# Kernel optimization log

Hardware: AMD Instinct MI355X
Metric: run time of the kernel (lower is better)

The kernel has to match this reference:

```python
import jax, jax.numpy as jnp
import numpy as np

B, SC, SV = 32, 300, 300
D, H, L, E, F = 512, 8, 6, 6, 1024
SEM = 768
VF = SEM + 1 + 1 + 6  # semantic + scene_offset + motion + emotion(6) = 776
CHORD, ROOT, ATTR = 159, 14, 14


def _ln(x, g, b, eps=1e-5):
    m = x.mean(-1, keepdims=True)
    v = ((x - m) ** 2).mean(-1, keepdims=True)
    return (x - m) / jnp.sqrt(v + eps) * g + b


def _mha(q_in, kv_in, qkv_w, qkv_b, ow, ob, mask=None):
    d = q_in.shape[-1]
    hd = d // H
    q = (q_in @ qkv_w[:d].T + qkv_b[:d]).reshape(q_in.shape[0], q_in.shape[1], H, hd)
    k = (kv_in @ qkv_w[d:2 * d].T + qkv_b[d:2 * d]).reshape(kv_in.shape[0], kv_in.shape[1], H, hd)
    v = (kv_in @ qkv_w[2 * d:].T + qkv_b[2 * d:]).reshape(kv_in.shape[0], kv_in.shape[1], H, hd)
    s = jnp.einsum('bqhd,bkhd->bhqk', q, k) / jnp.sqrt(jnp.asarray(hd, q.dtype))
    if mask is not None:
        s = s + mask
    a = jax.nn.softmax(s, axis=-1)
    o = jnp.einsum('bhqk,bkhd->bqhd', a, v).reshape(q_in.shape)
    return o @ ow.T + ob


def _moe(x, gw, gb, w1, b1, w2, b2, w3, b3):
    # top-2 routing over E experts, SwiGLU experts (GLUExpert)
    probs = jax.nn.softmax(x @ gw.T + gb, axis=-1)  # [B,S,E]
    topv, topi = jax.lax.top_k(probs, 2)
    wts = topv / topv.sum(-1, keepdims=True)
    full = (jax.nn.one_hot(topi, E, dtype=x.dtype) * wts[..., None]).sum(-2)  # [B,S,E]
    h = jax.nn.silu(jnp.einsum('bsd,edf->bsef', x, w1) + b1) * (jnp.einsum('bsd,edf->bsef', x, w2) + b2)
    eo = jnp.einsum('bsef,efd->bsed', h, w3) + b3
    return jnp.einsum('bse,bsed->bsd', full, eo)


def reference(x, x_root, x_attr, fsem, fkey, fscene, fmotion, femotion, emb_root, emb_attr, w_chord, b_chord, w_vis, b_vis, pos_c, pos_v, enc_qkv_w, enc_qkv_b, enc_ow, enc_ob, enc_ln1_g, enc_ln1_b, enc_ln2_g, enc_ln2_b, enc_gw, enc_gb, enc_w1, enc_b1, enc_w2, enc_b2, enc_w3, enc_b3, enc_fg, enc_fb, dec_sqkv_w, dec_sqkv_b, dec_sow, dec_sob, dec_cqkv_w, dec_cqkv_b, dec_cow, dec_cob, dec_ln1_g, dec_ln1_b, dec_ln2_g, dec_ln2_b, dec_ln3_g, dec_ln3_b, dec_gw, dec_gb, dec_w1, dec_b1, dec_w2, dec_b2, dec_w3, dec_b3, dec_fg, dec_fb, wout, bout):
    Bq, S = x_root.shape
    xe = emb_root[x_root] + emb_attr[x_attr]  # chord root + attr embeddings
    keyp = jnp.broadcast_to(fkey[:, 0][:, None, None], (Bq, S, 1)).astype(xe.dtype)
    xf = jnp.concatenate([xe, keyp], -1) @ w_chord.T + b_chord
    vfc = jnp.concatenate([fsem, fscene[..., None], fmotion[..., None], femotion], -1)  # [B,Sv,VF]
    vf = vfc @ w_vis.T + b_vis
    xf = xf + pos_c[:S][None]
    vf = vf + pos_v[:vf.shape[1]][None]
    causal = jnp.where(jnp.tril(jnp.ones((S, S), bool)), 0.0, jnp.finfo(xf.dtype).min).astype(xf.dtype)
    # encoder (post-norm): self-attn -> add&norm -> MoE -> add&norm
    h = vf
    for i in range(L):
        a = _mha(h, h, enc_qkv_w[i], enc_qkv_b[i], enc_ow[i], enc_ob[i])
        h = _ln(h + a, enc_ln1_g[i], enc_ln1_b[i])
        m = _moe(h, enc_gw[i], enc_gb[i], enc_w1[i], enc_b1[i], enc_w2[i], enc_b2[i], enc_w3[i], enc_b3[i])
        h = _ln(h + m, enc_ln2_g[i], enc_ln2_b[i])
    mem = _ln(h, enc_fg, enc_fb)
    # decoder: masked self-attn, cross-attn, MoE, each add&norm
    h = xf
    for i in range(L):
        a = _mha(h, h, dec_sqkv_w[i], dec_sqkv_b[i], dec_sow[i], dec_sob[i], causal)
        h = _ln(h + a, dec_ln1_g[i], dec_ln1_b[i])
        c = _mha(h, mem, dec_cqkv_w[i], dec_cqkv_b[i], dec_cow[i], dec_cob[i])
        h = _ln(h + c, dec_ln2_g[i], dec_ln2_b[i])
        m = _moe(h, dec_gw[i], dec_gb[i], dec_w1[i], dec_b1[i], dec_w2[i], dec_b2[i], dec_w3[i], dec_b3[i])
        h = _ln(h + m, dec_ln3_g[i], dec_ln3_b[i])
    h = _ln(h, dec_fg, dec_fb)
    return h @ wout.T + bout


def setup_inputs():
    key = jax.random.key(0)
    ks = iter(jax.random.split(key, 256))
    def nrm(*s):
        return jax.random.normal(next(ks), s, jnp.float32) * 0.02
    d = {}
    d['x'] = jax.random.randint(next(ks), (B, SC), 0, CHORD)
    d['x_root'] = jax.random.randint(next(ks), (B, SC), 0, ROOT)
    d['x_attr'] = jax.random.randint(next(ks), (B, SC), 0, ATTR)
    d['fsem'] = jax.random.normal(next(ks), (B, SV, SEM), jnp.float32)
    d['fkey'] = jax.random.uniform(next(ks), (B, 1), jnp.float32)
    d['fscene'] = jax.random.uniform(next(ks), (B, SV), jnp.float32)
    d['fmotion'] = jax.random.uniform(next(ks), (B, SV), jnp.float32)
    d['femotion'] = jax.random.uniform(next(ks), (B, SV, 6), jnp.float32)
    d['emb_root'] = nrm(ROOT, D)
    d['emb_attr'] = nrm(ATTR, D)
    d['w_chord'] = nrm(D, D + 1)
    d['b_chord'] = jnp.zeros((D,), jnp.float32)
    d['w_vis'] = nrm(D, VF)
    d['b_vis'] = jnp.zeros((D,), jnp.float32)
    d['pos_c'] = nrm(SC, D)
    d['pos_v'] = nrm(SV, D)
    def attn_params(pfx_qkv, pfx_o):
        d[pfx_qkv + '_w'] = nrm(L, 3 * D, D)
        d[pfx_qkv + '_b'] = jnp.zeros((L, 3 * D), jnp.float32)
        d[pfx_o + 'w'] = nrm(L, D, D)
        d[pfx_o + 'b'] = jnp.zeros((L, D), jnp.float32)
    attn_params('enc_qkv', 'enc_o')
    attn_params('dec_sqkv', 'dec_so')
    attn_params('dec_cqkv', 'dec_co')
    def moe_params(pfx):
        d[pfx + 'gw'] = nrm(L, E, D)
        d[pfx + 'gb'] = jnp.zeros((L, E), jnp.float32)
        d[pfx + 'w1'] = nrm(L, E, D, F)
        d[pfx + 'b1'] = jnp.zeros((L, E, F), jnp.float32)
        d[pfx + 'w2'] = nrm(L, E, D, F)
        d[pfx + 'b2'] = jnp.zeros((L, E, F), jnp.float32)
        d[pfx + 'w3'] = nrm(L, E, F, D)
        d[pfx + 'b3'] = jnp.zeros((L, E, D), jnp.float32)
    moe_params('enc_')
    moe_params('dec_')
    for n in ['enc_ln1', 'enc_ln2', 'dec_ln1', 'dec_ln2', 'dec_ln3']:
        d[n + '_g'] = jnp.ones((L, D), jnp.float32)
        d[n + '_b'] = jnp.zeros((L, D), jnp.float32)
    d['enc_fg'] = jnp.ones((D,), jnp.float32)
    d['enc_fb'] = jnp.zeros((D,), jnp.float32)
    d['dec_fg'] = jnp.ones((D,), jnp.float32)
    d['dec_fb'] = jnp.zeros((D,), jnp.float32)
    d['wout'] = nrm(CHORD, D)
    d['bout'] = jnp.zeros((CHORD,), jnp.float32)
    return d
```

## Files before the change

### kernel.cpp

```cpp
#include <hip/hip_runtime.h>

constexpr int B_ = 32, S_ = 300, D_ = 512, H_ = 8;
constexpr int L_ = 6, E_ = 6, F_ = 1024;
constexpr int CHORD_ = 159;
constexpr int R_ = B_ * S_;
constexpr int TD_ = 3 * D_;
constexpr int MT2_ = R_ / 128;
constexpr size_t WSCAP_ = (size_t)E_ * F_ * 512;

typedef short bfrag __attribute__((ext_vector_type(8)));
typedef float facc  __attribute__((ext_vector_type(4)));

static __device__ __forceinline__ facc mfma_(bfrag a, bfrag b, facc c) {
    return __builtin_amdgcn_mfma_f32_16x16x32_bf16(a, b, c, 0, 0, 0);
}

static __device__ __forceinline__ short f2bf_rne(float f) {
    unsigned u = __float_as_uint(f);
    return (short)((u + 0x7FFFu + ((u >> 16) & 1u)) >> 16);
}
static __device__ __forceinline__ void split2(float x, short& hi, short& lo) {
    unsigned u = __float_as_uint(x);
    hi = (short)(u >> 16);
    float fh = __uint_as_float(u & 0xFFFF0000u);
    lo = f2bf_rne(x - fh);
}

static __device__ __forceinline__ float2 blockReduce2(float s, float ss) {
    __shared__ float red[4][2];
    #pragma unroll
    for (int o = 32; o > 0; o >>= 1) { s += __shfl_down(s, o); ss += __shfl_down(ss, o); }
    const int wid = threadIdx.x >> 6, lane = threadIdx.x & 63;
    if (lane == 0) { red[wid][0] = s; red[wid][1] = ss; }
    __syncthreads();
    if (threadIdx.x == 0) {
        for (int w = 1; w < 4; ++w) { s += red[w][0]; ss += red[w][1]; }
        red[0][0] = s; red[0][1] = ss;
    }
    __syncthreads();
    return make_float2(red[0][0], red[0][1]);
}

__global__ void wsplit_kern(const float* __restrict__ src, short* __restrict__ dh, short* __restrict__ dl,
                            int N, int K, int Kp)
{
    const int idx = blockIdx.x * 256 + threadIdx.x;
    if (idx >= N * Kp) return;
    const int n = idx / Kp, k = idx - n * Kp;
    const float v = (k < K) ? src[(size_t)n * K + k] : 0.f;
    short sh, sl; split2(v, sh, sl);
    dh[idx] = sh; dl[idx] = sl;
}

__global__ __launch_bounds__(256) void tsplit_kern(const float* __restrict__ src,
                                                   short* __restrict__ dh, short* __restrict__ dl,
                                                   int K, int N)
{
    __shared__ float tile[32][33];
    const size_t eo = (size_t)blockIdx.z * K * N;
    const float* s = src + eo;
    short* oh = dh + eo;
    short* ol = dl + eo;
    const int kb = blockIdx.x * 32, nb = blockIdx.y * 32;
    const int c = threadIdx.x & 31, r0 = threadIdx.x >> 5;
    #pragma unroll
    for (int p = 0; p < 4; ++p) {
        const int r = r0 + p * 8;
        tile[r][c] = s[(size_t)(kb + r) * N + nb + c];
    }
    __syncthreads();
    #pragma unroll
    for (int p = 0; p < 4; ++p) {
        const int wn = r0 + p * 8;
        const float v = tile[c][wn];
        short sh, sl; split2(v, sh, sl);
        const size_t o = (size_t)(nb + wn) * K + kb + c;
        oh[o] = sh; ol[o] = sl;
    }
}

__global__ __launch_bounds__(256) void gemm_mfma(
    const short* __restrict__ Xh, const short* __restrict__ Xl,
    const short* __restrict__ Wh, const short* __restrict__ Wl, int Kp,
    const float* __restrict__ bias, const float* __restrict__ pos,
    float* __restrict__ Y, int ldy, int N,
    short* __restrict__ Yh, short* __restrict__ Yl)
{
    __shared__ __align__(16) short Ah[128][40], Al[128][40];
    __shared__ __align__(16) short Bh[128][40], Bl[128][40];
    const int m0 = blockIdx.x * 128, n0 = blockIdx.y * 128;
    const int tid = threadIdx.x;
    const int w = tid >> 6, l = tid & 63;
    const int wr = (w >> 1) * 64, wc = (w & 1) * 64;
    const facc zero = {0.f, 0.f, 0.f, 0.f};
    facc acc[4][4];
    #pragma unroll
    for (int i = 0; i < 4; ++i)
        #pragma unroll
        for (int j = 0; j < 4; ++j) acc[i][j] = zero;
    const int ar = tid >> 2, aks = (tid & 3) * 8;
    const int bc = tid >> 1, bk = (tid & 1) * 16;
    const bool bok = (n0 + bc) < N;
    const size_t a0 = (size_t)(m0 + ar) * Kp + aks;
    const size_t a1 = a0 + (size_t)64 * Kp;
    const size_t b0 = (size_t)(n0 + bc) * Kp + bk;
    const bfrag zf = {0, 0, 0, 0, 0, 0, 0, 0};
    bfrag pa0h, pa0l, pa1h, pa1l, pb0h, pb0l, pb1h, pb1l;
    auto LOAD = [&](int kc) {
        pa0h = *(const bfrag*)&Xh[a0 + kc];
        pa0l = *(const bfrag*)&Xl[a0 + kc];
        pa1h = *(const bfrag*)&Xh[a1 + kc];
        pa1l = *(const bfrag*)&Xl[a1 + kc];
        if (bok) {
            pb0h = *(const bfrag*)&Wh[b0 + kc];
            pb0l = *(const bfrag*)&Wl[b0 + kc];
            pb1h = *(const bfrag*)&Wh[b0 + kc + 8];
            pb1l = *(const bfrag*)&Wl[b0 + kc + 8];
        } else { pb0h = zf; pb0l = zf; pb1h = zf; pb1l = zf; }
    };
    LOAD(0);
    for (int kc = 0; kc < Kp; kc += 32) {
        *(bfrag*)&Ah[ar][aks]      = pa0h;  *(bfrag*)&Al[ar][aks]      = pa0l;
        *(bfrag*)&Ah[ar + 64][aks] = pa1h;  *(bfrag*)&Al[ar + 64][aks] = pa1l;
        *(bfrag*)&Bh[bc][bk]       = pb0h;  *(bfrag*)&Bl[bc][bk]       = pb0l;
        *(bfrag*)&Bh[bc][bk + 8]   = pb1h;  *(bfrag*)&Bl[bc][bk + 8]   = pb1l;
        __syncthreads();
        if (kc + 32 < Kp) LOAD(kc + 32);
        bfrag ah[4], al[4];
        #pragma unroll
        for (int i2 = 0; i2 < 4; ++i2) {
            ah[i2] = *(const bfrag*)&Ah[wr + i2 * 16 + (l & 15)][(l >> 4) * 8];
            al[i2] = *(const bfrag*)&Al[wr + i2 * 16 + (l & 15)][(l >> 4) * 8];
        }
        #pragma unroll
        for (int j = 0; j < 4; ++j) {
            const int cc = wc + j * 16 + (l & 15);
            const bfrag bh = *(const bfrag*)&Bh[cc][(l >> 4) * 8];
            const bfrag bl = *(const bfrag*)&Bl[cc][(l >> 4) * 8];
            #pragma unroll
            for (int i2 = 0; i2 < 4; ++i2) {
                acc[i2][j] = mfma_(ah[i2], bh, acc[i2][j]);
                acc[i2][j] = mfma_(al[i2], bh, acc[i2][j]);
                acc[i2][j] = mfma_(ah[i2], bl, acc[i2][j]);
            }
        }
        __syncthreads();
    }
    #pragma unroll
    for (int i2 = 0; i2 < 4; ++i2) {
        #pragma unroll
        for (int r = 0; r < 4; ++r) {
            const int m = m0 + wr + i2 * 16 + (l >> 4) * 4 + r;
            #pragma unroll
            for (int j = 0; j < 4; ++j) {
                const int n = n0 + wc + j * 16 + (l & 15);
                if (n < N) {
                    float y = acc[i2][j][r];
                    if (bias) y += bias[n];
                    if (pos)  y += pos[(size_t)(m % S_) * N + n];
                    Y[(size_t)m * ldy + n] = y;
                    if (Yh) {
                        short sh, sl; split2(y, sh, sl);
                        Yh[(size_t)m * ldy + n] = sh;
                        Yl[(size_t)m * ldy + n] = sl;
                    }
                }
            }
        }
    }
}

template<bool CAUSAL>
__global__ __launch_bounds__(320) void attn_kern(const float* __restrict__ qkv,
                                                 short* __restrict__ oh, short* __restrict__ ol)
{
    __shared__ float Ks[64][64];
    __shared__ float Vs[64][64];
    const int b = blockIdx.x >> 3, hh = blockIdx.x & 7;
    const int tid = threadIdx.x;
    const float* base = qkv + (size_t)b * S_ * TD_ + hh * 64;
    const bool act = tid < S_;
    float4 q4[16];
    if (act) {
        const float4* qp = (const float4*)(base + (size_t)tid * TD_);
        #pragma unroll
        for (int dd = 0; dd < 16; ++dd) q4[dd] = qp[dd];
    }
    float m = -3.0e38f, lsum = 0.f;
    float acc[64];
    #pragma unroll
    for (int d = 0; d < 64; ++d) acc[d] = 0.f;
    for (int j0 = 0; j0 < S_; j0 += 64) {
        const int tn = min(64, S_ - j0);
        __syncthreads();
        for (int idx = tid; idx < 64 * 64; idx += 320) {
            const int jj = idx >> 6, d = idx & 63;
            const bool ok = jj < tn;
            Ks[jj][d] = ok ? base[(size_t)(j0 + jj) * TD_ + D_ + d] : 0.f;
            Vs[jj][d] = ok ? base[(size_t)(j0 + jj) * TD_ + 2 * D_ + d] : 0.f;
        }
        __syncthreads();
        if (act) {
            const int jmax = CAUSAL ? min(tn, tid - j0 + 1) : tn;
            for (int jj = 0; jj < jmax; ++jj) {
                const float4* kp = (const float4*)Ks[jj];
                float s = 0.f;
                #pragma unroll
                for (int dd = 0; dd < 16; ++dd) {
                    const float4 kv = kp[dd];
                    s += q4[dd].x * kv.x + q4[dd].y * kv.y + q4[dd].z * kv.z + q4[dd].w * kv.w;
                }
                s *= 0.125f;
                float p;
                if (s > m) {
                    const float r = __expf(m - s);
                    lsum *= r;
                    #pragma unroll
                    for (int d = 0; d < 64; ++d) acc[d] *= r;
                    m = s; p = 1.f;
                } else {
                    p = __expf(s - m);
                }
                lsum += p;
                const float4* vp = (const float4*)Vs[jj];
                #pragma unroll
                for (int dd = 0; dd < 16; ++dd) {
                    const float4 vv = vp[dd];
                    acc[dd * 4 + 0] += p * vv.x; acc[dd * 4 + 1] += p * vv.y;
                    acc[dd * 4 + 2] += p * vv.z; acc[dd * 4 + 3] += p * vv.w;
                }
            }
        }
    }
    if (act) {
        const float inv = 1.f / lsum;
        const size_t ob = (size_t)(b * S_ + tid) * D_ + hh * 64;
        #pragma unroll
        for (int d = 0; d < 64; ++d) {
            short sh, sl; split2(acc[d] * inv, sh, sl);
            oh[ob + d] = sh; ol[ob + d] = sl;
        }
    }
}

__global__ __launch_bounds__(256) void add_ln_kern(float* __restrict__ h, const float* __restrict__ a,
    const float* __restrict__ g, const float* __restrict__ bb,
    short* __restrict__ dh, short* __restrict__ dl)
{
    const int r = blockIdx.x, tid = threadIdx.x;
    const size_t off = (size_t)r * D_;
    const float x0 = h[off + tid] + a[off + tid];
    const float x1 = h[off + tid + 256] + a[off + tid + 256];
    const float2 red = blockReduce2(x0 + x1, x0 * x0 + x1 * x1);
    const float mean = red.x * (1.f / D_);
    const float var = red.y * (1.f / D_) - mean * mean;
    const float rs = rsqrtf(var + 1e-5f);
    const float y0 = (x0 - mean) * rs * g[tid] + bb[tid];
    const float y1 = (x1 - mean) * rs * g[tid + 256] + bb[tid + 256];
    h[off + tid] = y0; h[off + tid + 256] = y1;
    short sh, sl;
    split2(y0, sh, sl); dh[off + tid] = sh;       dl[off + tid] = sl;
    split2(y1, sh, sl); dh[off + tid + 256] = sh; dl[off + tid + 256] = sl;
}

__global__ __launch_bounds__(256) void add2_ln_kern(float* __restrict__ h, const float* __restrict__ moeout,
    const float* __restrict__ g, const float* __restrict__ bb,
    short* __restrict__ dh, short* __restrict__ dl)
{
    const int r = blockIdx.x, tid = threadIdx.x;
    const size_t off = (size_t)r * D_;
    const size_t m0 = (size_t)(2 * r) * D_, m1 = (size_t)(2 * r + 1) * D_;
    const float x0 = h[off + tid]       + moeout[m0 + tid]       + moeout[m1 + tid];
    const float x1 = h[off + tid + 256] + moeout[m0 + tid + 256] + moeout[m1 + tid + 256];
    const float2 red = blockReduce2(x0 + x1, x0 * x0 + x1 * x1);
    const float mean = red.x * (1.f / D_);
    const float var = red.y * (1.f / D_) - mean * mean;
    const float rs = rsqrtf(var + 1e-5f);
    const float y0 = (x0 - mean) * rs * g[tid] + bb[tid];
    const float y1 = (x1 - mean) * rs * g[tid + 256] + bb[tid + 256];
    h[off + tid] = y0; h[off + tid + 256] = y1;
    short sh, sl;
    split2(y0, sh, sl); dh[off + tid] = sh;       dl[off + tid] = sl;
    split2(y1, sh, sl); dh[off + tid + 256] = sh; dl[off + tid + 256] = sl;
}

__global__ __launch_bounds__(256) void ln_kern(const float* __restrict__ src,
    const float* __restrict__ g, const float* __restrict__ bb,
    short* __restrict__ dh, short* __restrict__ dl)
{
    const int r = blockIdx.x, tid = threadIdx.x;
    const size_t off = (size_t)r * D_;
    const float x0 = src[off + tid];
    const float x1 = src[off + tid + 256];
    const float2 red = blockReduce2(x0 + x1, x0 * x0 + x1 * x1);
    const float mean = red.x * (1.f / D_);
    const float var = red.y * (1.f / D_) - mean * mean;
    const float rs = rsqrtf(var + 1e-5f);
    const float y0 = (x0 - mean) * rs * g[tid] + bb[tid];
    const float y1 = (x1 - mean) * rs * g[tid + 256] + bb[tid + 256];
    short sh, sl;
    split2(y0, sh, sl); dh[off + tid] = sh;       dl[off + tid] = sl;
    split2(y1, sh, sl); dh[off + tid + 256] = sh; dl[off + tid + 256] = sl;
}

__global__ void assemble_chord_split(const int* __restrict__ x_root, const int* __restrict__ x_attr,
    const float* __restrict__ emb_root, const float* __restrict__ emb_attr,
    const float* __restrict__ fkey, short* __restrict__ dh, short* __restrict__ dl)
{
    const int idx = blockIdx.x * 256 + threadIdx.x;
    if (idx >= R_ * 544) return;
    const int r = idx / 544, k = idx - r * 544;
    float v = 0.f;
    if (k < D_)       v = emb_root[x_root[r] * D_ + k] + emb_attr[x_attr[r] * D_ + k];
    else if (k == D_) v = fkey[r / S_];
    short sh, sl; split2(v, sh, sl);
    dh[idx] = sh; dl[idx] = sl;
}

__global__ void assemble_vis_split(const float* __restrict__ fsem, const float* __restrict__ fscene,
    const float* __restrict__ fmotion, const float* __restrict__ femotion,
    short* __restrict__ dh, short* __restrict__ dl)
{
    const int idx = blockIdx.x * 256 + threadIdx.x;
    if (idx >= R_ * 800) return;
    const int r = idx / 800, k = idx - r * 800;
    float v = 0.f;
    if (k < 768)       v = fsem[(size_t)r * 768 + k];
    else if (k == 768) v = fscene[r];
    else if (k == 769) v = fmotion[r];
    else if (k < 776)  v = femotion[(size_t)r * 6 + (k - 770)];
    short sh, sl; split2(v, sh, sl);
    dh[idx] = sh; dl[idx] = sl;
}

__global__ __launch_bounds__(256) void moe_route(const float* __restrict__ X,
    const float* __restrict__ gw, const float* __restrict__ gb,
    int* __restrict__ gcnt, int* __restrict__ gtok, float* __restrict__ gwt)
{
    const int t = blockIdx.x * 256 + threadIdx.x;
    if (t >= R_) return;
    float lg[E_];
    #pragma unroll
    for (int e = 0; e < E_; ++e) lg[e] = gb[e];
    const float* xp = X + (size_t)t * D_;
    for (int d = 0; d < D_; ++d) {
        const float xd = xp[d];
        #pragma unroll
        for (int e = 0; e < E_; ++e) lg[e] += xd * gw[e * D_ + d];
    }
    float mx = lg[0];
    #pragma unroll
    for (int e = 1; e < E_; ++e) mx = fmaxf(mx, lg[e]);
    float p[E_];
    #pragma unroll
    for (int e = 0; e < E_; ++e) p[e] = __expf(lg[e] - mx);
    int i1 = 0;
    #pragma unroll
    for (int e = 1; e < E_; ++e) if (p[e] > p[i1]) i1 = e;
    int i2 = (i1 == 0) ? 1 : 0;
    #pragma unroll
    for (int e = 0; e < E_; ++e) if (e != i1 && p[e] > p[i2]) i2 = e;
    const float denom = p[i1] + p[i2];
    const float w1 = p[i1] / denom, w2 = p[i2] / denom;
    int pos1 = atomicAdd(&gcnt[i1], 1);
    gtok[i1 * R_ + pos1] = t * 2;     gwt[i1 * R_ + pos1] = w1;
    int pos2 = atomicAdd(&gcnt[i2], 1);
    gtok[i2 * R_ + pos2] = t * 2 + 1; gwt[i2 * R_ + pos2] = w2;
}

__global__ __launch_bounds__(256) void moe_stageA(
    const short* __restrict__ Xh, const short* __restrict__ Xl,
    const short* __restrict__ W1h, const short* __restrict__ W1l,
    const short* __restrict__ W2h, const short* __restrict__ W2l,
    const float* __restrict__ b1, const float* __restrict__ b2,
    const int* __restrict__ gcnt, const int* __restrict__ gtok,
    short* __restrict__ H1h, short* __restrict__ H1l)
{
    const int e = blockIdx.x / MT2_, mt = blockIdx.x % MT2_;
    const int cnt = gcnt[e];
    const int m0t = mt * 128;
    if (m0t >= cnt) return;
    __shared__ int rid[128];
    __shared__ __align__(16) short Ah[128][40], Al[128][40];
    __shared__ __align__(16) short B1h[64][40], B1l[64][40], B2h[64][40], B2l[64][40];
    const int tid = threadIdx.x;
    if (tid < 128) rid[tid] = (m0t + tid < cnt) ? gtok[e * R_ + m0t + tid] : -1;
    __syncthreads();
    const int f0 = blockIdx.y * 64;
    const int w = tid >> 6, l = tid & 63;
    const int wr = (w >> 1) * 64, wf = (w & 1) * 32;
    const facc zero = {0.f, 0.f, 0.f, 0.f};
    facc acc1[4][2], acc2[4][2];
    #pragma unroll
    for (int i = 0; i < 4; ++i)
        #pragma unroll
        for (int j = 0; j < 2; ++j) { acc1[i][j] = zero; acc2[i][j] = zero; }
    const int ar = tid >> 2, aks = (tid & 3) * 8;
    const int r0 = rid[ar], r1 = rid[ar + 64];
    const size_t a0 = (r0 >= 0) ? ((size_t)(r0 >> 1) * 512 + aks) : 0;
    const size_t a1 = (r1 >= 0) ? ((size_t)(r1 >> 1) * 512 + aks) : 0;
    const int c = l;
    const short* bsrc = (w == 0) ? W1h : (w == 1) ? W1l : (w == 2) ? W2h : W2l;
    bsrc += ((size_t)e * F_ + f0 + c) * 512;
    short (*bdst)[40] = (w == 0) ? B1h : (w == 1) ? B1l : (w == 2) ? B2h : B2l;
    const bfrag zf = {0, 0, 0, 0, 0, 0, 0, 0};
    bfrag pa0h, pa0l, pa1h, pa1l, pb0, pb1, pb2, pb3;
    auto LOAD = [&](int kc) {
        pa0h = (r0 >= 0) ? *(const bfrag*)&Xh[a0 + kc] : zf;
        pa0l = (r0 >= 0) ? *(const bfrag*)&Xl[a0 + kc] : zf;
        pa1h = (r1 >= 0) ? *(const bfrag*)&Xh[a1 + kc] : zf;
        pa1l = (r1 >= 0) ? *(const bfrag*)&Xl[a1 + kc] : zf;
        pb0 = *(const bfrag*)&bsrc[kc];
        pb1 = *(const bfrag*)&bsrc[kc + 8];
        pb2 = *(const bfrag*)&bsrc[kc + 16];
        pb3 = *(const bfrag*)&bsrc[kc + 24];
    };
    LOAD(0);
    for (int kc = 0; kc < 512; kc += 32) {
        *(bfrag*)&Ah[ar][aks]      = pa0h;  *(bfrag*)&Al[ar][aks]      = pa0l;
        *(bfrag*)&Ah[ar + 64][aks] = pa1h;  *(bfrag*)&Al[ar + 64][aks] = pa1l;
        *(bfrag*)&bdst[c][0]  = pb0;  *(bfrag*)&bdst[c][8]  = pb1;
        *(bfrag*)&bdst[c][16] = pb2;  *(bfrag*)&bdst[c][24] = pb3;
        __syncthreads();
        if (kc + 32 < 512) LOAD(kc + 32);
        bfrag ah[4], al[4];
        #pragma unroll
        for (int i2 = 0; i2 < 4; ++i2) {
            ah[i2] = *(const bfrag*)&Ah[wr + i2 * 16 + (l & 15)][(l >> 4) * 8];
            al[i2] = *(const bfrag*)&Al[wr + i2 * 16 + (l & 15)][(l >> 4) * 8];
        }
        #pragma unroll
        for (int j = 0; j < 2; ++j) {
            const int fc = wf + j * 16 + (l & 15);
            const bfrag b1hf = *(const bfrag*)&B1h[fc][(l >> 4) * 8];
            const bfrag b1lf = *(const bfrag*)&B1l[fc][(l >> 4) * 8];
            const bfrag b2hf = *(const bfrag*)&B2h[fc][(l >> 4) * 8];
            const bfrag b2lf = *(const bfrag*)&B2l[fc][(l >> 4) * 8];
            #pragma unroll
            for (int i2 = 0; i2 < 4; ++i2) {
                acc1[i2][j] = mfma_(ah[i2], b1hf, acc1[i2][j]);
                acc1[i2][j] = mfma_(al[i2], b1hf, acc1[i2][j]);
                acc1[i2][j] = mfma_(ah[i2], b1lf, acc1[i2][j]);
                acc2[i2][j] = mfma_(ah[i2], b2hf, acc2[i2][j]);
                acc2[i2][j] = mfma_(al[i2], b2hf, acc2[i2][j]);
                acc2[i2][j] = mfma_(ah[i2], b2lf, acc2[i2][j]);
            }
        }
        __syncthreads();
    }
    #pragma unroll
    for (int i2 = 0; i2 < 4; ++i2) {
        #pragma unroll
        for (int r = 0; r < 4; ++r) {
            const int mi = wr + i2 * 16 + (l >> 4) * 4 + r;
            const int rr = rid[mi];
            if (rr < 0) continue;
            #pragma unroll
            for (int j = 0; j < 2; ++j) {
                const int f = f0 + wf + j * 16 + (l & 15);
                const float a1v = acc1[i2][j][r] + b1[e * F_ + f];
                const float a2v = acc2[i2][j][r] + b2[e * F_ + f];
                const float hv = (a1v / (1.f + __expf(-a1v))) * a2v;
                const size_t oi = (size_t)rr * F_ + f;
                short hs, ls; split2(hv, hs, ls);
                H1h[oi] = hs; H1l[oi] = ls;
            }
        }
    }
}

__global__ __launch_bounds__(256) void moe_stageB(
    const short* __restrict__ Xh, const short* __restrict__ Xl,
    const short* __restrict__ W3h, const short* __restrict__ W3l,
    const float* __restrict__ b3,
    const int* __restrict__ gcnt, const int* __restrict__ gtok, const float* __restrict__ gwt,
    float* __restrict__ moeout)
{
    const int e = blockIdx.x / MT2_, mt = blockIdx.x % MT2_;
    const int cnt = gcnt[e];
    const int m0t = mt * 128;
    if (m0t >= cnt) return;
    __shared__ int rid[128];
    __shared__ float wts[128];
    __shared__ __align__(16) short Ah[128][40], Al[128][40];
    __shared__ __align__(16) short Bh[128][40], Bl[128][40];
    const int tid = threadIdx.x;
    if (tid < 128) {
        rid[tid] = (m0t + tid < cnt) ? gtok[e * R_ + m0t + tid] : -1;
        wts[tid] = (m0t + tid < cnt) ? gwt[e * R_ + m0t + tid] : 0.f;
    }
    __syncthreads();
    const int n0 = blockIdx.y * 128;
    const int w = tid >> 6, l = tid & 63;
    const int wr = (w >> 1) * 64, wc = (w & 1) * 64;
    const facc zero = {0.f, 0.f, 0.f, 0.f};
    facc acc[4][4];
    #pragma unroll
    for (int i = 0; i < 4; ++i)
        #pragma unroll
        for (int j = 0; j < 4; ++j) acc[i][j] = zero;
    const int ar = tid >> 2, aks = (tid & 3) * 8;
    const int r0 = rid[ar], r1 = rid[ar + 64];
    const size_t a0 = (r0 >= 0) ? ((size_t)r0 * F_ + aks) : 0;
    const size_t a1 = (r1 >= 0) ? ((size_t)r1 * F_ + aks) : 0;
    const int bc = tid >> 1, bk = (tid & 1) * 16;
    const size_t b0 = ((size_t)e * 512 + n0 + bc) * 1024 + bk;
    const bfrag zf = {0, 0, 0, 0, 0, 0, 0, 0};
    bfrag pa0h, pa0l, pa1h, pa1l, pb0h, pb0l, pb1h, pb1l;
    auto LOAD = [&](int kc) {
        pa0h = (r0 >= 0) ? *(const bfrag*)&Xh[a0 + kc] : zf;
        pa0l = (r0 >= 0) ? *(const bfrag*)&Xl[a0 + kc] : zf;
        pa1h = (r1 >= 0) ? *(const bfrag*)&Xh[a1 + kc] : zf;
        pa1l = (r1 >= 0) ? *(const bfrag*)&Xl[a1 + kc] : zf;
        pb0h = *(const bfrag*)&W3h[b0 + kc];
        pb0l = *(const bfrag*)&W3l[b0 + kc];
        pb1h = *(const bfrag*)&W3h[b0 + kc + 8];
        pb1l = *(const bfrag*)&W3l[b0 + kc + 8];
    };
    LOAD(0);
    for (int kc = 0; kc < 1024; kc += 32) {
        *(bfrag*)&Ah[ar][aks]      = pa0h;  *(bfrag*)&Al[ar][aks]      = pa0l;
        *(bfrag*)&Ah[ar + 64][aks] = pa1h;  *(bfrag*)&Al[ar + 64][aks] = pa1l;
        *(bfrag*)&Bh[bc][bk]       = pb0h;  *(bfrag*)&Bl[bc][bk]       = pb0l;
        *(bfrag*)&Bh[bc][bk + 8]   = pb1h;  *(bfrag*)&Bl[bc][bk + 8]   = pb1l;
        __syncthreads();
        if (kc + 32 < 1024) LOAD(kc + 32);
        bfrag ah[4], al[4];
        #pragma unroll
        for (int i2 = 0; i2 < 4; ++i2) {
            ah[i2] = *(const bfrag*)&Ah[wr + i2 * 16 + (l & 15)][(l >> 4) * 8];
            al[i2] = *(const bfrag*)&Al[wr + i2 * 16 + (l & 15)][(l >> 4) * 8];
        }
        #pragma unroll
        for (int j = 0; j < 4; ++j) {
            const int cc = wc + j * 16 + (l & 15);
            const bfrag bh = *(const bfrag*)&Bh[cc][(l >> 4) * 8];
            const bfrag bl = *(const bfrag*)&Bl[cc][(l >> 4) * 8];
            #pragma unroll
            for (int i2 = 0; i2 < 4; ++i2) {
                acc[i2][j] = mfma_(ah[i2], bh, acc[i2][j]);
                acc[i2][j] = mfma_(al[i2], bh, acc[i2][j]);
                acc[i2][j] = mfma_(ah[i2], bl, acc[i2][j]);
            }
        }
        __syncthreads();
    }
    #pragma unroll
    for (int i2 = 0; i2 < 4; ++i2) {
        #pragma unroll
        for (int r = 0; r < 4; ++r) {
            const int mi = wr + i2 * 16 + (l >> 4) * 4 + r;
            const int rr = rid[mi];
            if (rr < 0) continue;
            const float wt = wts[mi];
            #pragma unroll
            for (int j = 0; j < 4; ++j) {
                const int n = n0 + wc + j * 16 + (l & 15);
                moeout[(size_t)rr * D_ + n] = wt * (acc[i2][j][r] + b3[e * D_ + n]);
            }
        }
    }
}

extern "C" void kernel_launch(void* const* d_in, const int* in_sizes, int n_in,
                              void* d_out, int out_size, void* d_ws, size_t ws_size,
                              hipStream_t stream) {
    (void)in_sizes; (void)n_in; (void)out_size; (void)ws_size;
    const int*   x_root    = (const int*)  d_in[1];
    const int*   x_attr    = (const int*)  d_in[2];
    const float* fsem      = (const float*)d_in[3];
    const float* fkey      = (const float*)d_in[4];
    const float* fscene    = (const float*)d_in[5];
    const float* fmotion   = (const float*)d_in[6];
    const float* femotion  = (const float*)d_in[7];
    const float* emb_root  = (const float*)d_in[8];
    const float* emb_attr  = (const float*)d_in[9];
    const float* w_chord   = (const float*)d_in[10];
    const float* b_chord   = (const float*)d_in[11];
    const float* w_vis     = (const float*)d_in[12];
    const float* b_vis     = (const float*)d_in[13];
    const float* pos_c     = (const float*)d_in[14];
    const float* pos_v     = (const float*)d_in[15];
    const float* enc_qkv_w = (const float*)d_in[16];
    const float* enc_qkv_b = (const float*)d_in[17];
    const float* enc_ow    = (const float*)d_in[18];
    const float* enc_ob    = (const float*)d_in[19];
    const float* dec_sqkv_w= (const float*)d_in[20];
    const float* dec_sqkv_b= (const float*)d_in[21];
    const float* dec_sow   = (const float*)d_in[22];
    const float* dec_sob   = (const float*)d_in[23];
    const float* dec_cqkv_w= (const float*)d_in[24];
    const float* dec_cqkv_b= (const float*)d_in[25];
    const float* dec_cow   = (const float*)d_in[26];
    const float* dec_cob   = (const float*)d_in[27];
    const float* enc_gw    = (const float*)d_in[28];
    const float* enc_gb    = (const float*)d_in[29];
    const float* enc_w1    = (const float*)d_in[30];
    const float* enc_b1    = (const float*)d_in[31];
    const float* enc_w2    = (const float*)d_in[32];
    const float* enc_b2    = (const float*)d_in[33];
    const float* enc_w3    = (const float*)d_in[34];
    const float* enc_b3    = (const float*)d_in[35];
    const float* dec_gw    = (const float*)d_in[36];
    const float* dec_gb    = (const float*)d_in[37];
    const float* dec_w1    = (const float*)d_in[38];
    const float* dec_b1    = (const float*)d_in[39];
    const float* dec_w2    = (const float*)d_in[40];
    const float* dec_b2    = (const float*)d_in[41];
    const float* dec_w3    = (const float*)d_in[42];
    const float* dec_b3    = (const float*)d_in[43];
    const float* enc_ln1_g = (const float*)d_in[44];
    const float* enc_ln1_b = (const float*)d_in[45];
    const float* enc_ln2_g = (const float*)d_in[46];
    const float* enc_ln2_b = (const float*)d_in[47];
    const float* dec_ln1_g = (const float*)d_in[48];
    const float* dec_ln1_b = (const float*)d_in[49];
    const float* dec_ln2_g = (const float*)d_in[50];
    const float* dec_ln2_b = (const float*)d_in[51];
    const float* dec_ln3_g = (const float*)d_in[52];
    const float* dec_ln3_b = (const float*)d_in[53];
    const float* enc_fg    = (const float*)d_in[54];
    const float* enc_fb    = (const float*)d_in[55];
    const float* dec_fg    = (const float*)d_in[56];
    const float* dec_fb    = (const float*)d_in[57];
    const float* wout      = (const float*)d_in[58];
    const float* bout      = (const float*)d_in[59];

    float* h    = (float*)d_ws;
    float* qkvb = h + (size_t)R_ * D_;
    short* PH   = (short*)(qkvb + (size_t)R_ * TD_);
    short* PL   = PH + (size_t)R_ * D_;
    short* MH   = PL + (size_t)R_ * D_;
    short* ML   = MH + (size_t)R_ * D_;
    short* H1H  = ML + (size_t)R_ * D_;
    short* H1L  = H1H + (size_t)2 * R_ * F_;
    short* WS0H = H1L + (size_t)2 * R_ * F_;
    short* WS0L = WS0H + WSCAP_;
    short* WS1H = WS0L + WSCAP_;
    short* WS1L = WS1H + WSCAP_;
    int*   gcnt = (int*)(WS1L + WSCAP_);
    int*   gtok = gcnt + 16;
    float* gwt  = (float*)(gtok + E_ * R_);
    short* AH   = (short*)qkvb;
    short* AL   = AH + (size_t)R_ * 800;

    auto wsplit = [&](const float* src, short* dh, short* dl, int N, int K, int Kp) {
        const int total = N * Kp;
        wsplit_kern<<<dim3((total + 255) / 256), dim3(256), 0, stream>>>(src, dh, dl, N, K, Kp);
    };
    auto tsplit = [&](const float* src, short* dh, short* dl, int K, int N) {
        tsplit_kern<<<dim3(K / 32, N / 32, E_), dim3(256), 0, stream>>>(src, dh, dl, K, N);
    };
    auto gemm = [&](const short* XhP, const short* XlP, int Kp,
                    const short* WhP, const short* WlP,
                    const float* bias, const float* pos,
                    float* Yf, int ldy, int N, short* Yh, short* Yl) {
        gemm_mfma<<<dim3(R_ / 128, (N + 127) / 128), dim3(256), 0, stream>>>(
            XhP, XlP, WhP, WlP, Kp, bias, pos, Yf, ldy, N, Yh, Yl);
    };
    auto run_moe = [&](const float* gw, const float* gb,
                       const float* w1, const float* b1, const float* w2, const float* b2,
                       const float* w3, const float* b3, const float* lng, const float* lnb) {
        hipMemsetAsync(gcnt, 0, 16 * sizeof(int), stream);
        moe_route<<<dim3((R_ + 255) / 256), dim3(256), 0, stream>>>(h, gw, gb, gcnt, gtok, gwt);
        tsplit(w1, WS0H, WS0L, D_, F_);
        tsplit(w2, WS1H, WS1L, D_, F_);
        moe_stageA<<<dim3(E_ * MT2_, F_ / 64), dim3(256), 0, stream>>>(
            PH, PL, WS0H, WS0L, WS1H, WS1L, b1, b2, gcnt, gtok, H1H, H1L);
        tsplit(w3, WS0H, WS0L, F_, D_);
        moe_stageB<<<dim3(E_ * MT2_, D_ / 128), dim3(256), 0, stream>>>(
            H1H, H1L, WS0H, WS0L, b3, gcnt, gtok, gwt, qkvb);
        add2_ln_kern<<<dim3(R_), dim3(256), 0, stream>>>(h, qkvb, lng, lnb, PH, PL);
    };

    wsplit(w_vis, WS0H, WS0L, D_, 776, 800);
    assemble_vis_split<<<dim3((R_ * 800 + 255) / 256), dim3(256), 0, stream>>>(
        fsem, fscene, fmotion, femotion, AH, AL);
    gemm(AH, AL, 800, WS0H, WS0L, b_vis, pos_v, h, D_, D_, PH, PL);

    for (int i = 0; i < L_; ++i) {
        wsplit(enc_qkv_w + (size_t)i * TD_ * D_, WS0H, WS0L, TD_, D_, D_);
        gemm(PH, PL, D_, WS0H, WS0L, enc_qkv_b + (size_t)i * TD_, nullptr, qkvb, TD_, TD_, nullptr, nullptr);
        attn_kern<false><<<dim3(B_ * H_), dim3(320), 0, stream>>>(qkvb, PH, PL);
        wsplit(enc_ow + (size_t)i * D_ * D_, WS0H, WS0L, D_, D_, D_);
        gemm(PH, PL, D_, WS0H, WS0L, enc_ob + (size_t)i * D_, nullptr, qkvb, D_, D_, nullptr, nullptr);
        add_ln_kern<<<dim3(R_), dim3(256), 0, stream>>>(h, qkvb, enc_ln1_g + i * D_, enc_ln1_b + i * D_, PH, PL);
        run_moe(enc_gw + (size_t)i * E_ * D_, enc_gb + (size_t)i * E_,
                enc_w1 + (size_t)i * E_ * D_ * F_, enc_b1 + (size_t)i * E_ * F_,
                enc_w2 + (size_t)i * E_ * D_ * F_, enc_b2 + (size_t)i * E_ * F_,
                enc_w3 + (size_t)i * E_ * F_ * D_, enc_b3 + (size_t)i * E_ * D_,
                enc_ln2_g + i * D_, enc_ln2_b + i * D_);
    }
    ln_kern<<<dim3(R_), dim3(256), 0, stream>>>(h, enc_fg, enc_fb, MH, ML);

    wsplit(w_chord, WS0H, WS0L, D_, 513, 544);
    assemble_chord_split<<<dim3((R_ * 544 + 255) / 256), dim3(256), 0, stream>>>(
        x_root, x_attr, emb_root, emb_attr, fkey, AH, AL);
    gemm(AH, AL, 544, WS0H, WS0L, b_chord, pos_c, h, D_, D_, PH, PL);

    for (int i = 0; i < L_; ++i) {
        wsplit(dec_sqkv_w + (size_t)i * TD_ * D_, WS0H, WS0L, TD_, D_, D_);
        gemm(PH, PL, D_, WS0H, WS0L, dec_sqkv_b + (size_t)i * TD_, nullptr, qkvb, TD_, TD_, nullptr, nullptr);
        attn_kern<true><<<dim3(B_ * H_), dim3(320), 0, stream>>>(qkvb, PH, PL);
        wsplit(dec_sow + (size_t)i * D_ * D_, WS0H, WS0L, D_, D_, D_);
        gemm(PH, PL, D_, WS0H, WS0L, dec_sob + (size_t)i * D_, nullptr, qkvb, D_, D_, nullptr, nullptr);
        add_ln_kern<<<dim3(R_), dim3(256), 0, stream>>>(h, qkvb, dec_ln1_g + i * D_, dec_ln1_b + i * D_, PH, PL);
        wsplit(dec_cqkv_w + (size_t)i * TD_ * D_, WS0H, WS0L, TD_, D_, D_);
        gemm(PH, PL, D_, WS0H, WS0L, dec_cqkv_b + (size_t)i * TD_, nullptr, qkvb, TD_, D_, nullptr, nullptr);
        gemm(MH, ML, D_, WS0H + (size_t)D_ * D_, WS0L + (size_t)D_ * D_,
             dec_cqkv_b + (size_t)i * TD_ + D_, nullptr, qkvb + D_, TD_, 2 * D_, nullptr, nullptr);
        attn_kern<false><<<dim3(B_ * H_), dim3(320), 0, stream>>>(qkvb, PH, PL);
        wsplit(dec_cow + (size_t)i * D_ * D_, WS0H, WS0L, D_, D_, D_);
        gemm(PH, PL, D_, WS0H, WS0L, dec_cob + (size_t)i * D_, nullptr, qkvb, D_, D_, nullptr, nullptr);
        add_ln_kern<<<dim3(R_), dim3(256), 0, stream>>>(h, qkvb, dec_ln2_g + i * D_, dec_ln2_b + i * D_, PH, PL);
        run_moe(dec_gw + (size_t)i * E_ * D_, dec_gb + (size_t)i * E_,
                dec_w1 + (size_t)i * E_ * D_ * F_, dec_b1 + (size_t)i * E_ * F_,
                dec_w2 + (size_t)i * E_ * D_ * F_, dec_b2 + (size_t)i * E_ * F_,
                dec_w3 + (size_t)i * E_ * F_ * D_, dec_b3 + (size_t)i * E_ * D_,
                dec_ln3_g + i * D_, dec_ln3_b + i * D_);
    }

    ln_kern<<<dim3(R_), dim3(256), 0, stream>>>(h, dec_fg, dec_fb, PH, PL);
    wsplit(wout, WS0H, WS0L, CHORD_, D_, D_);
    gemm(PH, PL, D_, WS0H, WS0L, bout, nullptr, (float*)d_out, CHORD_, CHORD_, nullptr, nullptr);
}
```

Baseline: 12.81 ms.

## Deepen GEMM K tiles, warp-per-row layernorm and routing, lazy softmax rescale

Every MFMA GEMM, the MoE stage kernels included, now stages 64-wide K chunks in LDS instead of 32, which halves the barrier count per tile and widens the global loads. LayerNorm, add+LayerNorm and MoE routing now give one wavefront per row, using float4 loads and wave shuffles in place of block reductions. The attention inner loop splits the dot product into four accumulators and rescales only when the running max grows by more than 8. The padded K of the input GEMMs grows to a multiple of 64, which means some extra zero-padding work, and the larger LDS tiles may reduce occupancy.

```diff
diff --git a/kernel.cpp b/kernel.cpp
--- a/kernel.cpp
+++ b/kernel.cpp
@@ -26,21 +26,6 @@
     lo = f2bf_rne(x - fh);
 }
 
-static __device__ __forceinline__ float2 blockReduce2(float s, float ss) {
-    __shared__ float red[4][2];
-    #pragma unroll
-    for (int o = 32; o > 0; o >>= 1) { s += __shfl_down(s, o); ss += __shfl_down(ss, o); }
-    const int wid = threadIdx.x >> 6, lane = threadIdx.x & 63;
-    if (lane == 0) { red[wid][0] = s; red[wid][1] = ss; }
-    __syncthreads();
-    if (threadIdx.x == 0) {
-        for (int w = 1; w < 4; ++w) { s += red[w][0]; ss += red[w][1]; }
-        red[0][0] = s; red[0][1] = ss;
-    }
-    __syncthreads();
-    return make_float2(red[0][0], red[0][1]);
-}
-
 __global__ void wsplit_kern(const float* __restrict__ src, short* __restrict__ dh, short* __restrict__ dl,
                             int N, int K, int Kp)
 {
@@ -86,8 +71,8 @@
     float* __restrict__ Y, int ldy, int N,
     short* __restrict__ Yh, short* __restrict__ Yl)
 {
-    __shared__ __align__(16) short Ah[128][40], Al[128][40];
-    __shared__ __align__(16) short Bh[128][40], Bl[128][40];
+    __shared__ __align__(16) short Ah[128][72], Al[128][72];
+    __shared__ __align__(16) short Bh[128][72], Bl[128][72];
     const int m0 = blockIdx.x * 128, n0 = blockIdx.y * 128;
     const int tid = threadIdx.x;
     const int w = tid >> 6, l = tid & 63;
@@ -98,50 +83,60 @@
     for (int i = 0; i < 4; ++i)
         #pragma unroll
         for (int j = 0; j < 4; ++j) acc[i][j] = zero;
-    const int ar = tid >> 2, aks = (tid & 3) * 8;
-    const int bc = tid >> 1, bk = (tid & 1) * 16;
+    const int ar = tid >> 1, ak = (tid & 1) * 32;
+    const int bc = tid >> 1, bk = (tid & 1) * 32;
     const bool bok = (n0 + bc) < N;
-    const size_t a0 = (size_t)(m0 + ar) * Kp + aks;
-    const size_t a1 = a0 + (size_t)64 * Kp;
-    const size_t b0 = (size_t)(n0 + bc) * Kp + bk;
+    const size_t abase = (size_t)(m0 + ar) * Kp + ak;
+    const size_t bbase = (size_t)(n0 + bc) * Kp + bk;
     const bfrag zf = {0, 0, 0, 0, 0, 0, 0, 0};
-    bfrag pa0h, pa0l, pa1h, pa1l, pb0h, pb0l, pb1h, pb1l;
+    bfrag pah[4], pal[4], pbh[4], pbl[4];
     auto LOAD = [&](int kc) {
-        pa0h = *(const bfrag*)&Xh[a0 + kc];
-        pa0l = *(const bfrag*)&Xl[a0 + kc];
-        pa1h = *(const bfrag*)&Xh[a1 + kc];
-        pa1l = *(const bfrag*)&Xl[a1 + kc];
+        #pragma unroll
+        for (int q = 0; q < 4; ++q) {
+            pah[q] = *(const bfrag*)&Xh[abase + kc + q * 8];
+            pal[q] = *(const bfrag*)&Xl[abase + kc + q * 8];
+        }
         if (bok) {
-            pb0h = *(const bfrag*)&Wh[b0 + kc];
-            pb0l = *(const bfrag*)&Wl[b0 + kc];
-            pb1h = *(const bfrag*)&Wh[b0 + kc + 8];
-            pb1l = *(const bfrag*)&Wl[b0 + kc + 8];
-        } else { pb0h = zf; pb0l = zf; pb1h = zf; pb1l = zf; }
+            #pragma unroll
+            for (int q = 0; q < 4; ++q) {
+                pbh[q] = *(const bfrag*)&Wh[bbase + kc + q * 8];
+                pbl[q] = *(const bfrag*)&Wl[bbase + kc + q * 8];
+            }
+        } else {
+            #pragma unroll
+            for (int q = 0; q < 4; ++q) { pbh[q] = zf; pbl[q] = zf; }
+        }
     };
     LOAD(0);
-    for (int kc = 0; kc < Kp; kc += 32) {
-        *(bfrag*)&Ah[ar][aks]      = pa0h;  *(bfrag*)&Al[ar][aks]      = pa0l;
-        *(bfrag*)&Ah[ar + 64][aks] = pa1h;  *(bfrag*)&Al[ar + 64][aks] = pa1l;
-        *(bfrag*)&Bh[bc][bk]       = pb0h;  *(bfrag*)&Bl[bc][bk]       = pb0l;
-        *(bfrag*)&Bh[bc][bk + 8]   = pb1h;  *(bfrag*)&Bl[bc][bk + 8]   = pb1l;
+    for (int kc = 0; kc < Kp; kc += 64) {
+        #pragma unroll
+        for (int q = 0; q < 4; ++q) {
+            *(bfrag*)&Ah[ar][ak + q * 8] = pah[q];
+            *(bfrag*)&Al[ar][ak + q * 8] = pal[q];
+            *(bfrag*)&Bh[bc][bk + q * 8] = pbh[q];
+            *(bfrag*)&Bl[bc][bk + q * 8] = pbl[q];
+        }
         __syncthreads();
-        if (kc + 32 < Kp) LOAD(kc + 32);
-        bfrag ah[4], al[4];
-        #pragma unroll
-        for (int i2 = 0; i2 < 4; ++i2) {
-            ah[i2] = *(const bfrag*)&Ah[wr + i2 * 16 + (l & 15)][(l >> 4) * 8];
-            al[i2] = *(const bfrag*)&Al[wr + i2 * 16 + (l & 15)][(l >> 4) * 8];
-        }
-        #pragma unroll
-        for (int j = 0; j < 4; ++j) {
-            const int cc = wc + j * 16 + (l & 15);
-            const bfrag bh = *(const bfrag*)&Bh[cc][(l >> 4) * 8];
-            const bfrag bl = *(const bfrag*)&Bl[cc][(l >> 4) * 8];
+        if (kc + 64 < Kp) LOAD(kc + 64);
+        #pragma unroll
+        for (int ks = 0; ks < 2; ++ks) {
+            bfrag ah[4], al[4];
             #pragma unroll
             for (int i2 = 0; i2 < 4; ++i2) {
-                acc[i2][j] = mfma_(ah[i2], bh, acc[i2][j]);
-                acc[i2][j] = mfma_(al[i2], bh, acc[i2][j]);
-                acc[i2][j] = mfma_(ah[i2], bl, acc[i2][j]);
+                ah[i2] = *(const bfrag*)&Ah[wr + i2 * 16 + (l & 15)][ks * 32 + (l >> 4) * 8];
+                al[i2] = *(const bfrag*)&Al[wr + i2 * 16 + (l & 15)][ks * 32 + (l >> 4) * 8];
+            }
+            #pragma unroll
+            for (int j = 0; j < 4; ++j) {
+                const int cc = wc + j * 16 + (l & 15);
+                const bfrag bh = *(const bfrag*)&Bh[cc][ks * 32 + (l >> 4) * 8];
+                const bfrag bl = *(const bfrag*)&Bl[cc][ks * 32 + (l >> 4) * 8];
+                #pragma unroll
+                for (int i2 = 0; i2 < 4; ++i2) {
+                    acc[i2][j] = mfma_(ah[i2], bh, acc[i2][j]);
+                    acc[i2][j] = mfma_(al[i2], bh, acc[i2][j]);
+                    acc[i2][j] = mfma_(ah[i2], bl, acc[i2][j]);
+                }
             }
         }
         __syncthreads();
@@ -204,23 +199,22 @@
             const int jmax = CAUSAL ? min(tn, tid - j0 + 1) : tn;
             for (int jj = 0; jj < jmax; ++jj) {
                 const float4* kp = (const float4*)Ks[jj];
-                float s = 0.f;
+                float s0 = 0.f, s1 = 0.f, s2 = 0.f, s3 = 0.f;
                 #pragma unroll
                 for (int dd = 0; dd < 16; ++dd) {
                     const float4 kv = kp[dd];
-                    s += q4[dd].x * kv.x + q4[dd].y * kv.y + q4[dd].z * kv.z + q4[dd].w * kv.w;
+                    s0 += q4[dd].x * kv.x; s1 += q4[dd].y * kv.y;
+                    s2 += q4[dd].z * kv.z; s3 += q4[dd].w * kv.w;
                 }
-                s *= 0.125f;
-                float p;
-                if (s > m) {
+                const float s = ((s0 + s1) + (s2 + s3)) * 0.125f;
+                if (s > m + 8.f) {
                     const float r = __expf(m - s);
                     lsum *= r;
                     #pragma unroll
                     for (int d = 0; d < 64; ++d) acc[d] *= r;
-                    m = s; p = 1.f;
-                } else {
-                    p = __expf(s - m);
+                    m = s;
                 }
+                const float p = __expf(s - m);
                 lsum += p;
                 const float4* vp = (const float4*)Vs[jj];
                 #pragma unroll
@@ -243,64 +237,88 @@
     }
 }
 
+static __device__ __forceinline__ float2 waveReduce2(float s, float ss) {
+    #pragma unroll
+    for (int o = 32; o > 0; o >>= 1) { s += __shfl_down(s, o); ss += __shfl_down(ss, o); }
+    s = __shfl(s, 0); ss = __shfl(ss, 0);
+    return make_float2(s, ss);
+}
+
+static __device__ __forceinline__ void ln_body(const float4 a, const float4 b,
+    const float* __restrict__ g, const float* __restrict__ bb, int lane,
+    float* __restrict__ outf, short* __restrict__ dh, short* __restrict__ dl, size_t off)
+{
+    const float sum = a.x + a.y + a.z + a.w + b.x + b.y + b.z + b.w;
+    const float ssq = a.x*a.x + a.y*a.y + a.z*a.z + a.w*a.w + b.x*b.x + b.y*b.y + b.z*b.z + b.w*b.w;
+    const float2 red = waveReduce2(sum, ssq);
+    const float mean = red.x * (1.f / D_);
+    const float var = red.y * (1.f / D_) - mean * mean;
+    const float rs = rsqrtf(var + 1e-5f);
+    const float4 ga = *(const float4*)&g[lane * 8];
+    const float4 gb4 = *(const float4*)&g[lane * 8 + 4];
+    const float4 ba = *(const float4*)&bb[lane * 8];
+    const float4 bb4 = *(const float4*)&bb[lane * 8 + 4];
+    float y[8];
+    y[0] = (a.x - mean) * rs * ga.x + ba.x;  y[1] = (a.y - mean) * rs * ga.y + ba.y;
+    y[2] = (a.z - mean) * rs * ga.z + ba.z;  y[3] = (a.w - mean) * rs * ga.w + ba.w;
+    y[4] = (b.x - mean) * rs * gb4.x + bb4.x; y[5] = (b.y - mean) * rs * gb4.y + bb4.y;
+    y[6] = (b.z - mean) * rs * gb4.z + bb4.z; y[7] = (b.w - mean) * rs * gb4.w + bb4.w;
+    if (outf) {
+        *(float4*)&outf[off + lane * 8]     = make_float4(y[0], y[1], y[2], y[3]);
+        *(float4*)&outf[off + lane * 8 + 4] = make_float4(y[4], y[5], y[6], y[7]);
+    }
+    bfrag vh, vl;
+    #pragma unroll
+    for (int i = 0; i < 8; ++i) { short sh, sl; split2(y[i], sh, sl); vh[i] = sh; vl[i] = sl; }
+    *(bfrag*)&dh[off + lane * 8] = vh;
+    *(bfrag*)&dl[off + lane * 8] = vl;
+}
+
 __global__ __launch_bounds__(256) void add_ln_kern(float* __restrict__ h, const float* __restrict__ a,
     const float* __restrict__ g, const float* __restrict__ bb,
     short* __restrict__ dh, short* __restrict__ dl)
 {
-    const int r = blockIdx.x, tid = threadIdx.x;
+    const int wid = threadIdx.x >> 6, lane = threadIdx.x & 63;
+    const int r = blockIdx.x * 4 + wid;
     const size_t off = (size_t)r * D_;
-    const float x0 = h[off + tid] + a[off + tid];
-    const float x1 = h[off + tid + 256] + a[off + tid + 256];
-    const float2 red = blockReduce2(x0 + x1, x0 * x0 + x1 * x1);
-    const float mean = red.x * (1.f / D_);
-    const float var = red.y * (1.f / D_) - mean * mean;
-    const float rs = rsqrtf(var + 1e-5f);
-    const float y0 = (x0 - mean) * rs * g[tid] + bb[tid];
-    const float y1 = (x1 - mean) * rs * g[tid + 256] + bb[tid + 256];
-    h[off + tid] = y0; h[off + tid + 256] = y1;
-    short sh, sl;
-    split2(y0, sh, sl); dh[off + tid] = sh;       dl[off + tid] = sl;
-    split2(y1, sh, sl); dh[off + tid + 256] = sh; dl[off + tid + 256] = sl;
+    float4 xa = *(const float4*)&h[off + lane * 8];
+    float4 xb = *(const float4*)&h[off + lane * 8 + 4];
+    const float4 aa = *(const float4*)&a[off + lane * 8];
+    const float4 ab = *(const float4*)&a[off + lane * 8 + 4];
+    xa.x += aa.x; xa.y += aa.y; xa.z += aa.z; xa.w += aa.w;
+    xb.x += ab.x; xb.y += ab.y; xb.z += ab.z; xb.w += ab.w;
+    ln_body(xa, xb, g, bb, lane, h, dh, dl, off);
 }
 
 __global__ __launch_bounds__(256) void add2_ln_kern(float* __restrict__ h, const float* __restrict__ moeout,
     const float* __restrict__ g, const float* __restrict__ bb,
     short* __restrict__ dh, short* __restrict__ dl)
 {
-    const int r = blockIdx.x, tid = threadIdx.x;
+    const int wid = threadIdx.x >> 6, lane = threadIdx.x & 63;
+    const int r = blockIdx.x * 4 + wid;
     const size_t off = (size_t)r * D_;
     const size_t m0 = (size_t)(2 * r) * D_, m1 = (size_t)(2 * r + 1) * D_;
-    const float x0 = h[off + tid]       + moeout[m0 + tid]       + moeout[m1 + tid];
-    const float x1 = h[off + tid + 256] + moeout[m0 + tid + 256] + moeout[m1 + tid + 256];
-    const float2 red = blockReduce2(x0 + x1, x0 * x0 + x1 * x1);
-    const float mean = red.x * (1.f / D_);
-    const float var = red.y * (1.f / D_) - mean * mean;
-    const float rs = rsqrtf(var + 1e-5f);
-    const float y0 = (x0 - mean) * rs * g[tid] + bb[tid];
-    const float y1 = (x1 - mean) * rs * g[tid + 256] + bb[tid + 256];
-    h[off + tid] = y0; h[off + tid + 256] = y1;
-    short sh, sl;
-    split2(y0, sh, sl); dh[off + tid] = sh;       dl[off + tid] = sl;
-    split2(y1, sh, sl); dh[off + tid + 256] = sh; dl[off + tid + 256] = sl;
+    float4 xa = *(const float4*)&h[off + lane * 8];
+    float4 xb = *(const float4*)&h[off + lane * 8 + 4];
+    const float4 p0a = *(const float4*)&moeout[m0 + lane * 8];
+    const float4 p0b = *(const float4*)&moeout[m0 + lane * 8 + 4];
+    const float4 p1a = *(const float4*)&moeout[m1 + lane * 8];
+    const float4 p1b = *(const float4*)&moeout[m1 + lane * 8 + 4];
+    xa.x += p0a.x + p1a.x; xa.y += p0a.y + p1a.y; xa.z += p0a.z + p1a.z; xa.w += p0a.w + p1a.w;
+    xb.x += p0b.x + p1b.x; xb.y += p0b.y + p1b.y; xb.z += p0b.z + p1b.z; xb.w += p0b.w + p1b.w;
+    ln_body(xa, xb, g, bb, lane, h, dh, dl, off);
 }
 
 __global__ __launch_bounds__(256) void ln_kern(const float* __restrict__ src,
     const float* __restrict__ g, const float* __restrict__ bb,
     short* __restrict__ dh, short* __restrict__ dl)
 {
-    const int r = blockIdx.x, tid = threadIdx.x;
+    const int wid = threadIdx.x >> 6, lane = threadIdx.x & 63;
+    const int r = blockIdx.x * 4 + wid;
     const size_t off = (size_t)r * D_;
-    const float x0 = src[off + tid];
-    const float x1 = src[off + tid + 256];
-    const float2 red = blockReduce2(x0 + x1, x0 * x0 + x1 * x1);
-    const float mean = red.x * (1.f / D_);
-    const float var = red.y * (1.f / D_) - mean * mean;
-    const float rs = rsqrtf(var + 1e-5f);
-    const float y0 = (x0 - mean) * rs * g[tid] + bb[tid];
-    const float y1 = (x1 - mean) * rs * g[tid + 256] + bb[tid + 256];
-    short sh, sl;
-    split2(y0, sh, sl); dh[off + tid] = sh;       dl[off + tid] = sl;
-    split2(y1, sh, sl); dh[off + tid + 256] = sh; dl[off + tid + 256] = sl;
+    const float4 xa = *(const float4*)&src[off + lane * 8];
+    const float4 xb = *(const float4*)&src[off + lane * 8 + 4];
+    ln_body(xa, xb, g, bb, lane, nullptr, dh, dl, off);
 }
 
 __global__ void assemble_chord_split(const int* __restrict__ x_root, const int* __restrict__ x_attr,
@@ -308,8 +326,8 @@
     const float* __restrict__ fkey, short* __restrict__ dh, short* __restrict__ dl)
 {
     const int idx = blockIdx.x * 256 + threadIdx.x;
-    if (idx >= R_ * 544) return;
-    const int r = idx / 544, k = idx - r * 544;
+    if (idx >= R_ * 576) return;
+    const int r = idx / 576, k = idx - r * 576;
     float v = 0.f;
     if (k < D_)       v = emb_root[x_root[r] * D_ + k] + emb_attr[x_attr[r] * D_ + k];
     else if (k == D_) v = fkey[r / S_];
@@ -322,8 +340,8 @@
     short* __restrict__ dh, short* __restrict__ dl)
 {
     const int idx = blockIdx.x * 256 + threadIdx.x;
-    if (idx >= R_ * 800) return;
-    const int r = idx / 800, k = idx - r * 800;
+    if (idx >= R_ * 832) return;
+    const int r = idx / 832, k = idx - r * 832;
     float v = 0.f;
     if (k < 768)       v = fsem[(size_t)r * 768 + k];
     else if (k == 768) v = fscene[r];
@@ -337,35 +355,45 @@
     const float* __restrict__ gw, const float* __restrict__ gb,
     int* __restrict__ gcnt, int* __restrict__ gtok, float* __restrict__ gwt)
 {
-    const int t = blockIdx.x * 256 + threadIdx.x;
-    if (t >= R_) return;
-    float lg[E_];
-    #pragma unroll
-    for (int e = 0; e < E_; ++e) lg[e] = gb[e];
-    const float* xp = X + (size_t)t * D_;
-    for (int d = 0; d < D_; ++d) {
-        const float xd = xp[d];
-        #pragma unroll
-        for (int e = 0; e < E_; ++e) lg[e] += xd * gw[e * D_ + d];
-    }
-    float mx = lg[0];
-    #pragma unroll
-    for (int e = 1; e < E_; ++e) mx = fmaxf(mx, lg[e]);
-    float p[E_];
-    #pragma unroll
-    for (int e = 0; e < E_; ++e) p[e] = __expf(lg[e] - mx);
-    int i1 = 0;
-    #pragma unroll
-    for (int e = 1; e < E_; ++e) if (p[e] > p[i1]) i1 = e;
-    int i2 = (i1 == 0) ? 1 : 0;
-    #pragma unroll
-    for (int e = 0; e < E_; ++e) if (e != i1 && p[e] > p[i2]) i2 = e;
-    const float denom = p[i1] + p[i2];
-    const float w1 = p[i1] / denom, w2 = p[i2] / denom;
-    int pos1 = atomicAdd(&gcnt[i1], 1);
-    gtok[i1 * R_ + pos1] = t * 2;     gwt[i1 * R_ + pos1] = w1;
-    int pos2 = atomicAdd(&gcnt[i2], 1);
-    gtok[i2 * R_ + pos2] = t * 2 + 1; gwt[i2 * R_ + pos2] = w2;
+    const int wid = threadIdx.x >> 6, lane = threadIdx.x & 63;
+    const int t = blockIdx.x * 4 + wid;
+    const float4 xa = *(const float4*)&X[(size_t)t * D_ + lane * 8];
+    const float4 xb = *(const float4*)&X[(size_t)t * D_ + lane * 8 + 4];
+    float p6[E_];
+    #pragma unroll
+    for (int e = 0; e < E_; ++e) {
+        const float4 ga = *(const float4*)&gw[e * D_ + lane * 8];
+        const float4 gb4 = *(const float4*)&gw[e * D_ + lane * 8 + 4];
+        p6[e] = xa.x*ga.x + xa.y*ga.y + xa.z*ga.z + xa.w*ga.w
+              + xb.x*gb4.x + xb.y*gb4.y + xb.z*gb4.z + xb.w*gb4.w;
+    }
+    #pragma unroll
+    for (int o = 32; o > 0; o >>= 1)
+        #pragma unroll
+        for (int e = 0; e < E_; ++e) p6[e] += __shfl_down(p6[e], o);
+    if (lane == 0) {
+        float lg[E_];
+        #pragma unroll
+        for (int e = 0; e < E_; ++e) lg[e] = p6[e] + gb[e];
+        float mx = lg[0];
+        #pragma unroll
+        for (int e = 1; e < E_; ++e) mx = fmaxf(mx, lg[e]);
+        float p[E_];
+        #pragma unroll
+        for (int e = 0; e < E_; ++e) p[e] = __expf(lg[e] - mx);
+        int i1 = 0;
+        #pragma unroll
+        for (int e = 1; e < E_; ++e) if (p[e] > p[i1]) i1 = e;
+        int i2 = (i1 == 0) ? 1 : 0;
+        #pragma unroll
+        for (int e = 0; e < E_; ++e) if (e != i1 && p[e] > p[i2]) i2 = e;
+        const float denom = p[i1] + p[i2];
+        const float w1 = p[i1] / denom, w2 = p[i2] / denom;
+        int pos1 = atomicAdd(&gcnt[i1], 1);
+        gtok[i1 * R_ + pos1] = t * 2;     gwt[i1 * R_ + pos1] = w1;
+        int pos2 = atomicAdd(&gcnt[i2], 1);
+        gtok[i2 * R_ + pos2] = t * 2 + 1; gwt[i2 * R_ + pos2] = w2;
+    }
 }
 
 __global__ __launch_bounds__(256) void moe_stageA(
@@ -381,8 +409,8 @@
     const int m0t = mt * 128;
     if (m0t >= cnt) return;
     __shared__ int rid[128];
-    __shared__ __align__(16) short Ah[128][40], Al[128][40];
-    __shared__ __align__(16) short B1h[64][40], B1l[64][40], B2h[64][40], B2l[64][40];
+    __shared__ __align__(16) short Ah[128][72], Al[128][72];
+    __shared__ __align__(16) short B1h[64][72], B1l[64][72], B2h[64][72], B2l[64][72];
     const int tid = threadIdx.x;
     if (tid < 128) rid[tid] = (m0t + tid < cnt) ? gtok[e * R_ + m0t + tid] : -1;
     __syncthreads();
@@ -395,55 +423,58 @@
     for (int i = 0; i < 4; ++i)
         #pragma unroll
         for (int j = 0; j < 2; ++j) { acc1[i][j] = zero; acc2[i][j] = zero; }
-    const int ar = tid >> 2, aks = (tid & 3) * 8;
-    const int r0 = rid[ar], r1 = rid[ar + 64];
-    const size_t a0 = (r0 >= 0) ? ((size_t)(r0 >> 1) * 512 + aks) : 0;
-    const size_t a1 = (r1 >= 0) ? ((size_t)(r1 >> 1) * 512 + aks) : 0;
-    const int c = l;
+    const int ar = tid >> 1, ak = (tid & 1) * 32;
+    const int r0 = rid[ar];
+    const size_t a0 = (r0 >= 0) ? ((size_t)(r0 >> 1) * 512 + ak) : 0;
     const short* bsrc = (w == 0) ? W1h : (w == 1) ? W1l : (w == 2) ? W2h : W2l;
-    bsrc += ((size_t)e * F_ + f0 + c) * 512;
-    short (*bdst)[40] = (w == 0) ? B1h : (w == 1) ? B1l : (w == 2) ? B2h : B2l;
+    bsrc += ((size_t)e * F_ + f0 + l) * 512;
+    short (*bdst)[72] = (w == 0) ? B1h : (w == 1) ? B1l : (w == 2) ? B2h : B2l;
     const bfrag zf = {0, 0, 0, 0, 0, 0, 0, 0};
-    bfrag pa0h, pa0l, pa1h, pa1l, pb0, pb1, pb2, pb3;
+    bfrag pah[4], pal[4], pb[8];
     auto LOAD = [&](int kc) {
-        pa0h = (r0 >= 0) ? *(const bfrag*)&Xh[a0 + kc] : zf;
-        pa0l = (r0 >= 0) ? *(const bfrag*)&Xl[a0 + kc] : zf;
-        pa1h = (r1 >= 0) ? *(const bfrag*)&Xh[a1 + kc] : zf;
-        pa1l = (r1 >= 0) ? *(const bfrag*)&Xl[a1 + kc] : zf;
-        pb0 = *(const bfrag*)&bsrc[kc];
-        pb1 = *(const bfrag*)&bsrc[kc + 8];
-        pb2 = *(const bfrag*)&bsrc[kc + 16];
-        pb3 = *(const bfrag*)&bsrc[kc + 24];
+        #pragma unroll
+        for (int q = 0; q < 4; ++q) {
+            pah[q] = (r0 >= 0) ? *(const bfrag*)&Xh[a0 + kc + q * 8] : zf;
+            pal[q] = (r0 >= 0) ? *(const bfrag*)&Xl[a0 + kc + q * 8] : zf;
+        }
+        #pragma unroll
+        for (int q = 0; q < 8; ++q) pb[q] = *(const bfrag*)&bsrc[kc + q * 8];
     };
     LOAD(0);
-    for (int kc = 0; kc < 512; kc += 32) {
-        *(bfrag*)&Ah[ar][aks]      = pa0h;  *(bfrag*)&Al[ar][aks]      = pa0l;
-        *(bfrag*)&Ah[ar + 64][aks] = pa1h;  *(bfrag*)&Al[ar + 64][aks] = pa1l;
-        *(bfrag*)&bdst[c][0]  = pb0;  *(bfrag*)&bdst[c][8]  = pb1;
-        *(bfrag*)&bdst[c][16] = pb2;  *(bfrag*)&bdst[c][24] = pb3;
+    for (int kc = 0; kc < 512; kc += 64) {
+        #pragma unroll
+        for (int q = 0; q < 4; ++q) {
+            *(bfrag*)&Ah[ar][ak + q * 8] = pah[q];
+            *(bfrag*)&Al[ar][ak + q * 8] = pal[q];
+        }
+        #pragma unroll
+        for (int q = 0; q < 8; ++q) *(bfrag*)&bdst[l][q * 8] = pb[q];
         __syncthreads();
-        if (kc + 32 < 512) LOAD(kc + 32);
-        bfrag ah[4], al[4];
-        #pragma unroll
-        for (int i2 = 0; i2 < 4; ++i2) {
-            ah[i2] = *(const bfrag*)&Ah[wr + i2 * 16 + (l & 15)][(l >> 4) * 8];
-            al[i2] = *(const bfrag*)&Al[wr + i2 * 16 + (l & 15)][(l >> 4) * 8];
-        }
-        #pragma unroll
-        for (int j = 0; j < 2; ++j) {
-            const int fc = wf + j * 16 + (l & 15);
-            const bfrag b1hf = *(const bfrag*)&B1h[fc][(l >> 4) * 8];
-            const bfrag b1lf = *(const bfrag*)&B1l[fc][(l >> 4) * 8];
-            const bfrag b2hf = *(const bfrag*)&B2h[fc][(l >> 4) * 8];
-            const bfrag b2lf = *(const bfrag*)&B2l[fc][(l >> 4) * 8];
+        if (kc + 64 < 512) LOAD(kc + 64);
+        #pragma unroll
+        for (int ks = 0; ks < 2; ++ks) {
+            bfrag ah[4], al[4];
             #pragma unroll
             for (int i2 = 0; i2 < 4; ++i2) {
-                acc1[i2][j] = mfma_(ah[i2], b1hf, acc1[i2][j]);
-                acc1[i2][j] = mfma_(al[i2], b1hf, acc1[i2][j]);
-                acc1[i2][j] = mfma_(ah[i2], b1lf, acc1[i2][j]);
-                acc2[i2][j] = mfma_(ah[i2], b2hf, acc2[i2][j]);
-                acc2[i2][j] = mfma_(al[i2], b2hf, acc2[i2][j]);
-                acc2[i2][j] = mfma_(ah[i2], b2lf, acc2[i2][j]);
+                ah[i2] = *(const bfrag*)&Ah[wr + i2 * 16 + (l & 15)][ks * 32 + (l >> 4) * 8];
+                al[i2] = *(const bfrag*)&Al[wr + i2 * 16 + (l & 15)][ks * 32 + (l >> 4) * 8];
+            }
+            #pragma unroll
+            for (int j = 0; j < 2; ++j) {
+                const int fc = wf + j * 16 + (l & 15);
+                const bfrag b1hf = *(const bfrag*)&B1h[fc][ks * 32 + (l >> 4) * 8];
+                const bfrag b1lf = *(const bfrag*)&B1l[fc][ks * 32 + (l >> 4) * 8];
+                const bfrag b2hf = *(const bfrag*)&B2h[fc][ks * 32 + (l >> 4) * 8];
+                const bfrag b2lf = *(const bfrag*)&B2l[fc][ks * 32 + (l >> 4) * 8];
+                #pragma unroll
+                for (int i2 = 0; i2 < 4; ++i2) {
+                    acc1[i2][j] = mfma_(ah[i2], b1hf, acc1[i2][j]);
+                    acc1[i2][j] = mfma_(al[i2], b1hf, acc1[i2][j]);
+                    acc1[i2][j] = mfma_(ah[i2], b1lf, acc1[i2][j]);
+                    acc2[i2][j] = mfma_(ah[i2], b2hf, acc2[i2][j]);
+                    acc2[i2][j] = mfma_(al[i2], b2hf, acc2[i2][j]);
+                    acc2[i2][j] = mfma_(ah[i2], b2lf, acc2[i2][j]);
+                }
             }
         }
         __syncthreads();
@@ -482,8 +513,8 @@
     if (m0t >= cnt) return;
     __shared__ int rid[128];
     __shared__ float wts[128];
-    __shared__ __align__(16) short Ah[128][40], Al[128][40];
-    __shared__ __align__(16) short Bh[128][40], Bl[128][40];
+    __shared__ __align__(16) short Ah[128][72], Al[128][72];
+    __shared__ __align__(16) short Bh[128][72], Bl[128][72];
     const int tid = threadIdx.x;
     if (tid < 128) {
         rid[tid] = (m0t + tid < cnt) ? gtok[e * R_ + m0t + tid] : -1;
@@ -499,48 +530,52 @@
     for (int i = 0; i < 4; ++i)
         #pragma unroll
         for (int j = 0; j < 4; ++j) acc[i][j] = zero;
-    const int ar = tid >> 2, aks = (tid & 3) * 8;
-    const int r0 = rid[ar], r1 = rid[ar + 64];
-    const size_t a0 = (r0 >= 0) ? ((size_t)r0 * F_ + aks) : 0;
-    const size_t a1 = (r1 >= 0) ? ((size_t)r1 * F_ + aks) : 0;
-    const int bc = tid >> 1, bk = (tid & 1) * 16;
+    const int ar = tid >> 1, ak = (tid & 1) * 32;
+    const int r0 = rid[ar];
+    const size_t a0 = (r0 >= 0) ? ((size_t)r0 * F_ + ak) : 0;
+    const int bc = tid >> 1, bk = (tid & 1) * 32;
     const size_t b0 = ((size_t)e * 512 + n0 + bc) * 1024 + bk;
     const bfrag zf = {0, 0, 0, 0, 0, 0, 0, 0};
-    bfrag pa0h, pa0l, pa1h, pa1l, pb0h, pb0l, pb1h, pb1l;
+    bfrag pah[4], pal[4], pbh[4], pbl[4];
     auto LOAD = [&](int kc) {
-        pa0h = (r0 >= 0) ? *(const bfrag*)&Xh[a0 + kc] : zf;
-        pa0l = (r0 >= 0) ? *(const bfrag*)&Xl[a0 + kc] : zf;
-        pa1h = (r1 >= 0) ? *(const bfrag*)&Xh[a1 + kc] : zf;
-        pa1l = (r1 >= 0) ? *(const bfrag*)&Xl[a1 + kc] : zf;
-        pb0h = *(const bfrag*)&W3h[b0 + kc];
-        pb0l = *(const bfrag*)&W3l[b0 + kc];
-        pb1h = *(const bfrag*)&W3h[b0 + kc + 8];
-        pb1l = *(const bfrag*)&W3l[b0 + kc + 8];
+        #pragma unroll
+        for (int q = 0; q < 4; ++q) {
+            pah[q] = (r0 >= 0) ? *(const bfrag*)&Xh[a0 + kc + q * 8] : zf;
+            pal[q] = (r0 >= 0) ? *(const bfrag*)&Xl[a0 + kc + q * 8] : zf;
+            pbh[q] = *(const bfrag*)&W3h[b0 + kc + q * 8];
+            pbl[q] = *(const bfrag*)&W3l[b0 + kc + q * 8];
+        }
     };
     LOAD(0);
-    for (int kc = 0; kc < 1024; kc += 32) {
-        *(bfrag*)&Ah[ar][aks]      = pa0h;  *(bfrag*)&Al[ar][aks]      = pa0l;
-        *(bfrag*)&Ah[ar + 64][aks] = pa1h;  *(bfrag*)&Al[ar + 64][aks] = pa1l;
-        *(bfrag*)&Bh[bc][bk]       = pb0h;  *(bfrag*)&Bl[bc][bk]       = pb0l;
-        *(bfrag*)&Bh[bc][bk + 8]   = pb1h;  *(bfrag*)&Bl[bc][bk + 8]   = pb1l;
+    for (int kc = 0; kc < 1024; kc += 64) {
+        #pragma unroll
+        for (int q = 0; q < 4; ++q) {
+            *(bfrag*)&Ah[ar][ak + q * 8] = pah[q];
+            *(bfrag*)&Al[ar][ak + q * 8] = pal[q];
+            *(bfrag*)&Bh[bc][bk + q * 8] = pbh[q];
+            *(bfrag*)&Bl[bc][bk + q * 8] = pbl[q];
+        }
         __syncthreads();
-        if (kc + 32 < 1024) LOAD(kc + 32);
-        bfrag ah[4], al[4];
-        #pragma unroll
-        for (int i2 = 0; i2 < 4; ++i2) {
-            ah[i2] = *(const bfrag*)&Ah[wr + i2 * 16 + (l & 15)][(l >> 4) * 8];
-            al[i2] = *(const bfrag*)&Al[wr + i2 * 16 + (l & 15)][(l >> 4) * 8];
-        }
-        #pragma unroll
-        for (int j = 0; j < 4; ++j) {
-            const int cc = wc + j * 16 + (l & 15);
-            const bfrag bh = *(const bfrag*)&Bh[cc][(l >> 4) * 8];
-            const bfrag bl = *(const bfrag*)&Bl[cc][(l >> 4) * 8];
+        if (kc + 64 < 1024) LOAD(kc + 64);
+        #pragma unroll
+        for (int ks = 0; ks < 2; ++ks) {
+            bfrag ah[4], al[4];
             #pragma unroll
             for (int i2 = 0; i2 < 4; ++i2) {
-                acc[i2][j] = mfma_(ah[i2], bh, acc[i2][j]);
-                acc[i2][j] = mfma_(al[i2], bh, acc[i2][j]);
-                acc[i2][j] = mfma_(ah[i2], bl, acc[i2][j]);
+                ah[i2] = *(const bfrag*)&Ah[wr + i2 * 16 + (l & 15)][ks * 32 + (l >> 4) * 8];
+                al[i2] = *(const bfrag*)&Al[wr + i2 * 16 + (l & 15)][ks * 32 + (l >> 4) * 8];
+            }
+            #pragma unroll
+            for (int j = 0; j < 4; ++j) {
+                const int cc = wc + j * 16 + (l & 15);
+                const bfrag bh = *(const bfrag*)&Bh[cc][ks * 32 + (l >> 4) * 8];
+                const bfrag bl = *(const bfrag*)&Bl[cc][ks * 32 + (l >> 4) * 8];
+                #pragma unroll
+                for (int i2 = 0; i2 < 4; ++i2) {
+                    acc[i2][j] = mfma_(ah[i2], bh, acc[i2][j]);
+                    acc[i2][j] = mfma_(al[i2], bh, acc[i2][j]);
+                    acc[i2][j] = mfma_(ah[i2], bl, acc[i2][j]);
+                }
             }
         }
         __syncthreads();
@@ -642,7 +677,7 @@
     int*   gtok = gcnt + 16;
     float* gwt  = (float*)(gtok + E_ * R_);
     short* AH   = (short*)qkvb;
-    short* AL   = AH + (size_t)R_ * 800;
+    short* AL   = AH + (size_t)R_ * 832;
 
     auto wsplit = [&](const float* src, short* dh, short* dl, int N, int K, int Kp) {
         const int total = N * Kp;
@@ -662,7 +697,7 @@
                        const float* w1, const float* b1, const float* w2, const float* b2,
                        const float* w3, const float* b3, const float* lng, const float* lnb) {
         hipMemsetAsync(gcnt, 0, 16 * sizeof(int), stream);
-        moe_route<<<dim3((R_ + 255) / 256), dim3(256), 0, stream>>>(h, gw, gb, gcnt, gtok, gwt);
+        moe_route<<<dim3(R_ / 4), dim3(256), 0, stream>>>(h, gw, gb, gcnt, gtok, gwt);
         tsplit(w1, WS0H, WS0L, D_, F_);
         tsplit(w2, WS1H, WS1L, D_, F_);
         moe_stageA<<<dim3(E_ * MT2_, F_ / 64), dim3(256), 0, stream>>>(
@@ -670,13 +705,13 @@
         tsplit(w3, WS0H, WS0L, F_, D_);
         moe_stageB<<<dim3(E_ * MT2_, D_ / 128), dim3(256), 0, stream>>>(
             H1H, H1L, WS0H, WS0L, b3, gcnt, gtok, gwt, qkvb);
-        add2_ln_kern<<<dim3(R_), dim3(256), 0, stream>>>(h, qkvb, lng, lnb, PH, PL);
+        add2_ln_kern<<<dim3(R_ / 4), dim3(256), 0, stream>>>(h, qkvb, lng, lnb, PH, PL);
     };
 
-    wsplit(w_vis, WS0H, WS0L, D_, 776, 800);
-    assemble_vis_split<<<dim3((R_ * 800 + 255) / 256), dim3(256), 0, stream>>>(
+    wsplit(w_vis, WS0H, WS0L, D_, 776, 832);
+    assemble_vis_split<<<dim3((R_ * 832 + 255) / 256), dim3(256), 0, stream>>>(
         fsem, fscene, fmotion, femotion, AH, AL);
-    gemm(AH, AL, 800, WS0H, WS0L, b_vis, pos_v, h, D_, D_, PH, PL);
+    gemm(AH, AL, 832, WS0H, WS0L, b_vis, pos_v, h, D_, D_, PH, PL);
 
     for (int i = 0; i < L_; ++i) {
         wsplit(enc_qkv_w + (size_t)i * TD_ * D_, WS0H, WS0L, TD_, D_, D_);
@@ -684,19 +719,19 @@
         attn_kern<false><<<dim3(B_ * H_), dim3(320), 0, stream>>>(qkvb, PH, PL);
         wsplit(enc_ow + (size_t)i * D_ * D_, WS0H, WS0L, D_, D_, D_);
         gemm(PH, PL, D_, WS0H, WS0L, enc_ob + (size_t)i * D_, nullptr, qkvb, D_, D_, nullptr, nullptr);
-        add_ln_kern<<<dim3(R_), dim3(256), 0, stream>>>(h, qkvb, enc_ln1_g + i * D_, enc_ln1_b + i * D_, PH, PL);
+        add_ln_kern<<<dim3(R_ / 4), dim3(256), 0, stream>>>(h, qkvb, enc_ln1_g + i * D_, enc_ln1_b + i * D_, PH, PL);
         run_moe(enc_gw + (size_t)i * E_ * D_, enc_gb + (size_t)i * E_,
                 enc_w1 + (size_t)i * E_ * D_ * F_, enc_b1 + (size_t)i * E_ * F_,
                 enc_w2 + (size_t)i * E_ * D_ * F_, enc_b2 + (size_t)i * E_ * F_,
                 enc_w3 + (size_t)i * E_ * F_ * D_, enc_b3 + (size_t)i * E_ * D_,
                 enc_ln2_g + i * D_, enc_ln2_b + i * D_);
     }
-    ln_kern<<<dim3(R_), dim3(256), 0, stream>>>(h, enc_fg, enc_fb, MH, ML);
-
-    wsplit(w_chord, WS0H, WS0L, D_, 513, 544);
-    assemble_chord_split<<<dim3((R_ * 544 + 255) / 256), dim3(256), 0, stream>>>(
+    ln_kern<<<dim3(R_ / 4), dim3(256), 0, stream>>>(h, enc_fg, enc_fb, MH, ML);
+
+    wsplit(w_chord, WS0H, WS0L, D_, 513, 576);
+    assemble_chord_split<<<dim3((R_ * 576 + 255) / 256), dim3(256), 0, stream>>>(
         x_root, x_attr, emb_root, emb_attr, fkey, AH, AL);
-    gemm(AH, AL, 544, WS0H, WS0L, b_chord, pos_c, h, D_, D_, PH, PL);
+    gemm(AH, AL, 576, WS0H, WS0L, b_chord, pos_c, h, D_, D_, PH, PL);
 
     for (int i = 0; i < L_; ++i) {
         wsplit(dec_sqkv_w + (size_t)i * TD_ * D_, WS0H, WS0L, TD_, D_, D_);
@@ -704,7 +739,7 @@
         attn_kern<true><<<dim3(B_ * H_), dim3(320), 0, stream>>>(qkvb, PH, PL);
         wsplit(dec_sow + (size_t)i * D_ * D_, WS0H, WS0L, D_, D_, D_);
         gemm(PH, PL, D_, WS0H, WS0L, dec_sob + (size_t)i * D_, nullptr, qkvb, D_, D_, nullptr, nullptr);
-        add_ln_kern<<<dim3(R_), dim3(256), 0, stream>>>(h, qkvb, dec_ln1_g + i * D_, dec_ln1_b + i * D_, PH, PL);
+        add_ln_kern<<<dim3(R_ / 4), dim3(256), 0, stream>>>(h, qkvb, dec_ln1_g + i * D_, dec_ln1_b + i * D_, PH, PL);
         wsplit(dec_cqkv_w + (size_t)i * TD_ * D_, WS0H, WS0L, TD_, D_, D_);
         gemm(PH, PL, D_, WS0H, WS0L, dec_cqkv_b + (size_t)i * TD_, nullptr, qkvb, TD_, D_, nullptr, nullptr);
         gemm(MH, ML, D_, WS0H + (size_t)D_ * D_, WS0L + (size_t)D_ * D_,
@@ -712,7 +747,7 @@
         attn_kern<false><<<dim3(B_ * H_), dim3(320), 0, stream>>>(qkvb, PH, PL);
         wsplit(dec_cow + (size_t)i * D_ * D_, WS0H, WS0L, D_, D_, D_);
         gemm(PH, PL, D_, WS0H, WS0L, dec_cob + (size_t)i * D_, nullptr, qkvb, D_, D_, nullptr, nullptr);
-        add_ln_kern<<<dim3(R_), dim3(256), 0, stream>>>(h, qkvb, dec_ln2_g + i * D_, dec_ln2_b + i * D_, PH, PL);
+        add_ln_kern<<<dim3(R_ / 4), dim3(256), 0, stream>>>(h, qkvb, dec_ln2_g + i * D_, dec_ln2_b + i * D_, PH, PL);
         run_moe(dec_gw + (size_t)i * E_ * D_, dec_gb + (size_t)i * E_,
                 dec_w1 + (size_t)i * E_ * D_ * F_, dec_b1 + (size_t)i * E_ * F_,
                 dec_w2 + (size_t)i * E_ * D_ * F_, dec_b2 + (size_t)i * E_ * F_,
@@ -720,7 +755,7 @@
                 dec_ln3_g + i * D_, dec_ln3_b + i * D_);
     }
 
-    ln_kern<<<dim3(R_), dim3(256), 0, stream>>>(h, dec_fg, dec_fb, PH, PL);
+    ln_kern<<<dim3(R_ / 4), dim3(256), 0, stream>>>(h, dec_fg, dec_fb, PH, PL);
     wsplit(wout, WS0H, WS0L, CHORD_, D_, D_);
     gemm(PH, PL, D_, WS0H, WS0L, bout, nullptr, (float*)d_out, CHORD_, CHORD_, nullptr, nullptr);
 }
```

Result: slower. 15.53 ms (+21.2%).
